# Kernel optimization log

Measured on AMD Instinct MI355X. Metric: run time of the kernel, lower is better.

## Reference

```python
import jax, jax.numpy as jnp
import numpy as np

N = 100000
E = 1600000
IN, HID, OUT = 128, 64, 32


def setup_inputs() -> dict:
    key = jax.random.key(0)
    ks = jax.random.split(key, 8)
    x = jax.random.normal(ks[0], (N, IN), dtype=jnp.float32)
    edge_index = jax.random.randint(ks[1], (2, E), 0, N, dtype=jnp.int32)
    eps = jax.random.normal(ks[2], (N, OUT), dtype=jnp.float32)
    W1 = jax.random.normal(ks[3], (IN, HID), dtype=jnp.float32) / np.sqrt(IN)
    b1 = jnp.zeros((HID,), jnp.float32)
    Wmu = jax.random.normal(ks[4], (HID, OUT), dtype=jnp.float32) / np.sqrt(HID)
    bmu = jnp.zeros((OUT,), jnp.float32)
    Wls = jax.random.normal(ks[5], (HID, OUT), dtype=jnp.float32) / np.sqrt(HID)
    bls = jnp.zeros((OUT,), jnp.float32)
    return dict(x=x, edge_index=edge_index, eps=eps, W1=W1, b1=b1,
                Wmu=Wmu, bmu=bmu, Wls=Wls, bls=bls)


def reference(x, edge_index, eps, W1, b1, Wmu, bmu, Wls, bls):
    n = x.shape[0]
    src, dst = edge_index[0], edge_index[1]
    # GCN with self-loops and symmetric normalization (PyG GCNConv default)
    loop = jnp.arange(n, dtype=src.dtype)
    s = jnp.concatenate([src, loop])   # [E+N]
    d = jnp.concatenate([dst, loop])
    deg = jax.ops.segment_sum(jnp.ones_like(s, jnp.float32), d, num_segments=n)
    dis = jax.lax.rsqrt(jnp.maximum(deg, 1.0))  # deg >= 1 due to self-loops
    norm = dis[s] * dis[d]                       # [E+N]

    def gcn_conv(h, W, b):
        h = h @ W                                # transform first (small dim)
        msg = h[s] * norm[:, None]               # gather over edges
        return jax.ops.segment_sum(msg, d, num_segments=n) + b

    h = jax.nn.relu(gcn_conv(x, W1, b1))
    # F.normalize(h, p=2, dim=-1)
    h = h / jnp.maximum(jnp.linalg.norm(h, axis=-1, keepdims=True), 1e-12)
    mu = gcn_conv(h, Wmu, bmu)
    logstd = gcn_conv(h, Wls, bls)
    # reparametrize (training mode): mu + randn * exp(clamp(logstd, -10, 10))
    z = mu + eps * jnp.exp(jnp.clip(logstd, -10.0, 10.0))
    # decode: sigmoid(<z_i, z_j>) over original edges
    adj_pred = jax.nn.sigmoid(jnp.sum(z[src] * z[dst], axis=1))
    return adj_pred, mu, logstd
```

## Files before the change

### kernel.cpp

```cpp
#include <hip/hip_runtime.h>
#include <hip/hip_fp16.h>

#define NN 100000
#define NE 1600000
#define W_BKT 128
#define NB_BKT ((NN + W_BKT - 1) / W_BKT)
#define TILE_E 16384
#define NT ((NE + TILE_E - 1) / TILE_E)
#define STAGE_CAP 4352

typedef _Float16 half2v __attribute__((ext_vector_type(2)));
typedef _Float16 half8v __attribute__((ext_vector_type(8)));
typedef float float2v __attribute__((ext_vector_type(2)));
typedef float float4v __attribute__((ext_vector_type(4)));


__global__ __launch_bounds__(256) void k_cnt(const int* __restrict__ dst,
                                             int* __restrict__ counts) {
    __shared__ int hc[NB_BKT];
    int tid = threadIdx.x;
    for (int i = tid; i < NB_BKT; i += 256) hc[i] = 0;
    __syncthreads();
    int base = blockIdx.x * TILE_E;
    int lim = base + TILE_E; if (lim > NE) lim = NE;
    for (int e = base + tid; e < lim; e += 256)
        atomicAdd(&hc[dst[e] >> 7], 1);
    __syncthreads();
    for (int i = tid; i < NB_BKT; i += 256)
        counts[blockIdx.x * NB_BKT + i] = hc[i];
}

__global__ __launch_bounds__(1024) void k_bscan(const int* __restrict__ counts,
                                                int* __restrict__ bucket_base) {
    __shared__ int buf[1024];
    int tid = threadIdx.x;
    int total = 0;
    if (tid < NB_BKT)
        for (int t = 0; t < NT; ++t) total += counts[t * NB_BKT + tid];
    buf[tid] = total;
    __syncthreads();
    for (int off = 1; off < 1024; off <<= 1) {
        int v = (tid >= off) ? buf[tid - off] : 0;
        __syncthreads();
        buf[tid] += v;
        __syncthreads();
    }
    if (tid < NB_BKT) bucket_base[tid] = buf[tid] - total;
    if (tid == 0) bucket_base[NB_BKT] = NE;
}

__global__ __launch_bounds__(256) void k_offs(const int* __restrict__ bucket_base,
                                              int* __restrict__ counts) {
    int b = blockIdx.x * 256 + threadIdx.x;
    if (b >= NB_BKT) return;
    int off = bucket_base[b];
    for (int t = 0; t < NT; ++t) {
        int c = counts[t * NB_BKT + b];
        counts[t * NB_BKT + b] = off;
        off += c;
    }
}

__global__ __launch_bounds__(256) void k_place(const int* __restrict__ src,
                                               const int* __restrict__ dst,
                                               const int* __restrict__ counts,
                                               int* __restrict__ ebuf) {
    __shared__ int cur[NB_BKT];
    int tid = threadIdx.x;
    for (int i = tid; i < NB_BKT; i += 256)
        cur[i] = counts[blockIdx.x * NB_BKT + i];
    __syncthreads();
    int base = blockIdx.x * TILE_E;
    int lim = base + TILE_E; if (lim > NE) lim = NE;
    for (int e = base + tid; e < lim; e += 256) {
        int s = src[e], d = dst[e];
        int pos = atomicAdd(&cur[d >> 7], 1);
        ebuf[pos] = (s << 7) | (d & 127);
    }
}

__global__ __launch_bounds__(256) void k_build(const int* __restrict__ bucket_base,
                                               const int* __restrict__ ebuf,
                                               int* __restrict__ csr_src,
                                               int* __restrict__ row_ptr,
                                               float* __restrict__ dis) {
    __shared__ int deg[W_BKT];
    __shared__ int pre[W_BKT];
    __shared__ int cur[W_BKT];
    __shared__ int stage[STAGE_CAP];
    int b = blockIdx.x;
    int tid = threadIdx.x;
    int beg = bucket_base[b], end = bucket_base[b + 1];
    int n = end - beg;
    if (tid < W_BKT) deg[tid] = 0;
    __syncthreads();
    bool fits = (n <= STAGE_CAP);
    if (fits) {
        for (int i = tid; i < n; i += 256) {
            int val = ebuf[beg + i];
            stage[i] = val;
            atomicAdd(&deg[val & 127], 1);
        }
    } else {
        for (int i = tid; i < n; i += 256)
            atomicAdd(&deg[ebuf[beg + i] & 127], 1);
    }
    __syncthreads();
    if (tid < W_BKT) pre[tid] = deg[tid];
    __syncthreads();
    for (int off = 1; off < W_BKT; off <<= 1) {
        int v = (tid >= off && tid < W_BKT) ? pre[tid - off] : 0;
        __syncthreads();
        if (tid < W_BKT) pre[tid] += v;
        __syncthreads();
    }
    if (tid < W_BKT) {
        int v = b * W_BKT + tid;
        int rp = beg + pre[tid] - deg[tid];
        if (v < NN) {
            row_ptr[v] = rp;
            dis[v] = rsqrtf((float)(1 + deg[tid]));
        }
        cur[tid] = rp;
    }
    if (b == NB_BKT - 1 && tid == 0) row_ptr[NN] = NE;
    __syncthreads();
    if (fits) {
        for (int i = tid; i < n; i += 256) {
            int val = stage[i];
            int pos = atomicAdd(&cur[val & 127], 1);
            csr_src[pos] = val >> 7;
        }
    } else {
        for (int i = tid; i < n; i += 256) {
            int val = ebuf[beg + i];
            int pos = atomicAdd(&cur[val & 127], 1);
            csr_src[pos] = val >> 7;
        }
    }
}


__global__ __launch_bounds__(256) void k_wprep(const float* __restrict__ W1,
                                               const float* __restrict__ Wmu,
                                               const float* __restrict__ Wls,
                                               _Float16* __restrict__ wf1h,
                                               _Float16* __restrict__ wf1l,
                                               _Float16* __restrict__ wf2h,
                                               _Float16* __restrict__ wf2l) {
    int tid = threadIdx.x;
    for (int f = tid; f < 4 * 4 * 64; f += 256) {
        int lane = f & 63;
        int kc = (f >> 6) & 3;
        int ct = f >> 8;
        int col = ct * 16 + (lane & 15);
        int k0 = kc * 32 + (lane >> 4) * 8;
#pragma unroll
        for (int j = 0; j < 8; ++j) {
            float w = W1[(k0 + j) * 64 + col];
            _Float16 hi = (_Float16)w;
            wf1h[f * 8 + j] = hi;
            wf1l[f * 8 + j] = (_Float16)(w - (float)hi);
        }
    }
    for (int f = tid; f < 4 * 2 * 64; f += 256) {
        int lane = f & 63;
        int kc = (f >> 6) & 1;
        int ct = f >> 7;
        int col = ct * 16 + (lane & 15);
        int k0 = kc * 32 + (lane >> 4) * 8;
#pragma unroll
        for (int j = 0; j < 8; ++j) {
            int k = k0 + j;
            float w = (col < 32) ? Wmu[k * 32 + col] : Wls[k * 32 + (col - 32)];
            _Float16 hi = (_Float16)w;
            wf2h[f * 8 + j] = hi;
            wf2l[f * 8 + j] = (_Float16)(w - (float)hi);
        }
    }
}

__device__ __forceinline__ void split8(const float4 a, const float4 b,
                                       half8v& hi, half8v& lo) {
    float v[8] = {a.x, a.y, a.z, a.w, b.x, b.y, b.z, b.w};
#pragma unroll
    for (int i = 0; i < 8; ++i) {
        _Float16 h = (_Float16)v[i];
        hi[i] = h;
        lo[i] = (_Float16)(v[i] - (float)h);
    }
}

__global__ __launch_bounds__(256) void k_gemm1(const float* __restrict__ x,
                                               const _Float16* __restrict__ wf1h,
                                               const _Float16* __restrict__ wf1l,
                                               const float* __restrict__ dis,
                                               _Float16* __restrict__ t1) {
    int tid = threadIdx.x;
    int lane = tid & 63;
    int wv = tid >> 6;
    int wrow = blockIdx.x * 64 + wv * 16;
    int cl = lane & 15, kg = lane >> 4;
    const half8v* Bh = (const half8v*)wf1h;
    const half8v* Bl = (const half8v*)wf1l;
    float4v acc[4] = {};
    int r = wrow + cl;
    long rr = (r < NN) ? r : (NN - 1);
    const float4* xp = (const float4*)(x + rr * 128);
#pragma unroll
    for (int kc = 0; kc < 4; ++kc) {
        float4 xa = xp[kc * 8 + kg * 2];
        float4 xb = xp[kc * 8 + kg * 2 + 1];
        half8v ah, al;
        split8(xa, xb, ah, al);
#pragma unroll
        for (int ct = 0; ct < 4; ++ct) {
            half8v bh = Bh[(ct * 4 + kc) * 64 + lane];
            half8v bl = Bl[(ct * 4 + kc) * 64 + lane];
            acc[ct] = __builtin_amdgcn_mfma_f32_16x16x32_f16(ah, bh, acc[ct], 0, 0, 0);
            acc[ct] = __builtin_amdgcn_mfma_f32_16x16x32_f16(al, bh, acc[ct], 0, 0, 0);
            acc[ct] = __builtin_amdgcn_mfma_f32_16x16x32_f16(ah, bl, acc[ct], 0, 0, 0);
        }
    }
#pragma unroll
    for (int j = 0; j < 4; ++j) {
        int row = wrow + kg * 4 + j;
        if (row < NN) {
            float dv = dis[row];
#pragma unroll
            for (int ct = 0; ct < 4; ++ct)
                t1[(long)row * 64 + ct * 16 + cl] = (_Float16)(acc[ct][j] * dv);
        }
    }
}

__global__ __launch_bounds__(256) void k_gemm2(const float* __restrict__ h,
                                               const _Float16* __restrict__ wf2h,
                                               const _Float16* __restrict__ wf2l,
                                               const float* __restrict__ dis,
                                               _Float16* __restrict__ t2) {
    int tid = threadIdx.x;
    int lane = tid & 63;
    int wv = tid >> 6;
    int wrow = blockIdx.x * 64 + wv * 16;
    int cl = lane & 15, kg = lane >> 4;
    const half8v* Bh = (const half8v*)wf2h;
    const half8v* Bl = (const half8v*)wf2l;
    float4v acc[4] = {};
    int r = wrow + cl;
    long rr = (r < NN) ? r : (NN - 1);
    const float4* hp = (const float4*)(h + rr * 64);
#pragma unroll
    for (int kc = 0; kc < 2; ++kc) {
        float4 xa = hp[kc * 8 + kg * 2];
        float4 xb = hp[kc * 8 + kg * 2 + 1];
        half8v ah, al;
        split8(xa, xb, ah, al);
#pragma unroll
        for (int ct = 0; ct < 4; ++ct) {
            half8v bh = Bh[(ct * 2 + kc) * 64 + lane];
            half8v bl = Bl[(ct * 2 + kc) * 64 + lane];
            acc[ct] = __builtin_amdgcn_mfma_f32_16x16x32_f16(ah, bh, acc[ct], 0, 0, 0);
            acc[ct] = __builtin_amdgcn_mfma_f32_16x16x32_f16(al, bh, acc[ct], 0, 0, 0);
            acc[ct] = __builtin_amdgcn_mfma_f32_16x16x32_f16(ah, bl, acc[ct], 0, 0, 0);
        }
    }
#pragma unroll
    for (int j = 0; j < 4; ++j) {
        int row = wrow + kg * 4 + j;
        if (row < NN) {
            float dv = dis[row];
#pragma unroll
            for (int ct = 0; ct < 4; ++ct)
                t2[(long)row * 64 + ct * 16 + cl] = (_Float16)(acc[ct][j] * dv);
        }
    }
}


__global__ __launch_bounds__(256) void k_agg1(const half2v* __restrict__ tv,
                                              const int* __restrict__ row_ptr,
                                              const int* __restrict__ csr_src,
                                              const float* __restrict__ dis,
                                              const float* __restrict__ b1,
                                              float* __restrict__ h) {
    int lane = threadIdx.x & 63;
    int j2 = lane & 31;
    int v = blockIdx.x * 8 + (threadIdx.x >> 6) * 2 + (lane >> 5);
    int beg = row_ptr[v], end = row_ptr[v + 1];
    float acc0 = 0.f, acc1 = 0.f;
    for (int base = beg; base < end; base += 32) {
        int cnt = end - base; if (cnt > 32) cnt = 32;
        int idx = 0;
        if (j2 < cnt) idx = csr_src[base + j2];
        int k = 0;
        for (; k + 8 <= cnt; k += 8) {
            int s0 = __shfl(idx, k, 32),     s1 = __shfl(idx, k + 1, 32),
                s2 = __shfl(idx, k + 2, 32), s3 = __shfl(idx, k + 3, 32),
                s4 = __shfl(idx, k + 4, 32), s5 = __shfl(idx, k + 5, 32),
                s6 = __shfl(idx, k + 6, 32), s7 = __shfl(idx, k + 7, 32);
            half2v r0 = tv[s0 * 32 + j2];
            half2v r1 = tv[s1 * 32 + j2];
            half2v r2 = tv[s2 * 32 + j2];
            half2v r3 = tv[s3 * 32 + j2];
            half2v r4 = tv[s4 * 32 + j2];
            half2v r5 = tv[s5 * 32 + j2];
            half2v r6 = tv[s6 * 32 + j2];
            half2v r7 = tv[s7 * 32 + j2];
            acc0 += (float)r0.x; acc1 += (float)r0.y;
            acc0 += (float)r1.x; acc1 += (float)r1.y;
            acc0 += (float)r2.x; acc1 += (float)r2.y;
            acc0 += (float)r3.x; acc1 += (float)r3.y;
            acc0 += (float)r4.x; acc1 += (float)r4.y;
            acc0 += (float)r5.x; acc1 += (float)r5.y;
            acc0 += (float)r6.x; acc1 += (float)r6.y;
            acc0 += (float)r7.x; acc1 += (float)r7.y;
        }
        for (; k < cnt; ++k) {
            int s = __shfl(idx, k, 32);
            half2v r = tv[s * 32 + j2];
            acc0 += (float)r.x; acc1 += (float)r.y;
        }
    }
    float dv = dis[v];
    half2v rv = tv[v * 32 + j2];
    float val0 = dv * (acc0 + (float)rv.x) + b1[2 * j2];
    float val1 = dv * (acc1 + (float)rv.y) + b1[2 * j2 + 1];
    val0 = fmaxf(val0, 0.0f);
    val1 = fmaxf(val1, 0.0f);
    float ss = val0 * val0 + val1 * val1;
#pragma unroll
    for (int m = 1; m < 32; m <<= 1) ss += __shfl_xor(ss, m);
    float scale = 1.0f / fmaxf(sqrtf(ss), 1e-12f);
    float2v* h2 = (float2v*)h;
    float2v hv; hv.x = val0 * scale; hv.y = val1 * scale;
    h2[v * 32 + j2] = hv;
}

__global__ __launch_bounds__(256) void k_agg2(const half2v* __restrict__ tv,
                                              const int* __restrict__ row_ptr,
                                              const int* __restrict__ csr_src,
                                              const float* __restrict__ dis,
                                              const float* __restrict__ bmu,
                                              const float* __restrict__ bls,
                                              const float* __restrict__ eps,
                                              float* __restrict__ mu,
                                              float* __restrict__ ls,
                                              _Float16* __restrict__ zh) {
    int lane = threadIdx.x & 63;
    int j2 = lane & 31;
    int v = blockIdx.x * 8 + (threadIdx.x >> 6) * 2 + (lane >> 5);
    int beg = row_ptr[v], end = row_ptr[v + 1];
    float acc0 = 0.f, acc1 = 0.f;
    for (int base = beg; base < end; base += 32) {
        int cnt = end - base; if (cnt > 32) cnt = 32;
        int idx = 0;
        if (j2 < cnt) idx = csr_src[base + j2];
        int k = 0;
        for (; k + 8 <= cnt; k += 8) {
            int s0 = __shfl(idx, k, 32),     s1 = __shfl(idx, k + 1, 32),
                s2 = __shfl(idx, k + 2, 32), s3 = __shfl(idx, k + 3, 32),
                s4 = __shfl(idx, k + 4, 32), s5 = __shfl(idx, k + 5, 32),
                s6 = __shfl(idx, k + 6, 32), s7 = __shfl(idx, k + 7, 32);
            half2v r0 = tv[s0 * 32 + j2];
            half2v r1 = tv[s1 * 32 + j2];
            half2v r2 = tv[s2 * 32 + j2];
            half2v r3 = tv[s3 * 32 + j2];
            half2v r4 = tv[s4 * 32 + j2];
            half2v r5 = tv[s5 * 32 + j2];
            half2v r6 = tv[s6 * 32 + j2];
            half2v r7 = tv[s7 * 32 + j2];
            acc0 += (float)r0.x; acc1 += (float)r0.y;
            acc0 += (float)r1.x; acc1 += (float)r1.y;
            acc0 += (float)r2.x; acc1 += (float)r2.y;
            acc0 += (float)r3.x; acc1 += (float)r3.y;
            acc0 += (float)r4.x; acc1 += (float)r4.y;
            acc0 += (float)r5.x; acc1 += (float)r5.y;
            acc0 += (float)r6.x; acc1 += (float)r6.y;
            acc0 += (float)r7.x; acc1 += (float)r7.y;
        }
        for (; k < cnt; ++k) {
            int s = __shfl(idx, k, 32);
            half2v r = tv[s * 32 + j2];
            acc0 += (float)r.x; acc1 += (float)r.y;
        }
    }
    float dv = dis[v];
    half2v rv = tv[v * 32 + j2];
    float bb0 = (j2 < 16) ? bmu[2 * j2]     : bls[2 * j2 - 32];
    float bb1 = (j2 < 16) ? bmu[2 * j2 + 1] : bls[2 * j2 - 31];
    float val0 = dv * (acc0 + (float)rv.x) + bb0;
    float val1 = dv * (acc1 + (float)rv.y) + bb1;
    float o0 = __shfl_xor(val0, 16);
    float o1 = __shfl_xor(val1, 16);
    float2v* mu2 = (float2v*)mu;
    float2v* ls2 = (float2v*)ls;
    half2v* z2  = (half2v*)zh;
    const float2* e2 = (const float2*)eps;
    if (j2 < 16) {
        float2v mv; mv.x = val0; mv.y = val1;
        __builtin_nontemporal_store(mv, &mu2[v * 16 + j2]);
        float2 ev = e2[v * 16 + j2];
        float l0 = fminf(fmaxf(o0, -10.0f), 10.0f);
        float l1 = fminf(fmaxf(o1, -10.0f), 10.0f);
        half2v zw;
        zw.x = (_Float16)(val0 + ev.x * expf(l0));
        zw.y = (_Float16)(val1 + ev.y * expf(l1));
        z2[v * 16 + j2] = zw;
    } else {
        float2v lv; lv.x = val0; lv.y = val1;
        __builtin_nontemporal_store(lv, &ls2[v * 16 + (j2 - 16)]);
    }
}

__global__ __launch_bounds__(256) void k_decode(const _Float16* __restrict__ zh,
                                                const int* __restrict__ src,
                                                const int* __restrict__ dst,
                                                float* __restrict__ out) {
    long t = (long)blockIdx.x * 256 + threadIdx.x;
    long e = t >> 2; int l = (int)(t & 3);
    if (e >= NE) return;
    int s = src[e], d = dst[e];
    const half8v* z8 = (const half8v*)zh;
    half8v a = z8[s * 4 + l];
    half8v b = z8[d * 4 + l];
    float p = 0.f;
#pragma unroll
    for (int i = 0; i < 8; ++i) p += (float)a[i] * (float)b[i];
    p += __shfl_xor(p, 1);
    p += __shfl_xor(p, 2);
    if (l == 0) out[e] = 1.0f / (1.0f + expf(-p));
}

extern "C" void kernel_launch(void* const* d_in, const int* in_sizes, int n_in,
                              void* d_out, int out_size, void* d_ws, size_t ws_size,
                              hipStream_t stream) {
    const float* x   = (const float*)d_in[0];
    const int*   ei  = (const int*)d_in[1];
    const float* eps = (const float*)d_in[2];
    const float* W1  = (const float*)d_in[3];
    const float* b1  = (const float*)d_in[4];
    const float* Wmu = (const float*)d_in[5];
    const float* bmu = (const float*)d_in[6];
    const float* Wls = (const float*)d_in[7];
    const float* bls = (const float*)d_in[8];
    const int* src = ei;
    const int* dst = ei + NE;

    float* out = (float*)d_out;
    float* adj = out;
    float* mu  = out + NE;
    float* ls  = mu + (long)NN * 32;

    float* dis      = (float*)d_ws;
    int*   row_ptr  = (int*)(dis + NN);
    int*   bucket_base = row_ptr + 100004;
    int*   counts   = bucket_base + 784;
    int*   ebuf     = counts + 76640;
    int*   csr_src  = ebuf + NE;
    _Float16* t     = (_Float16*)(csr_src + NE);
    float* h        = (float*)(t + (long)NN * 64);
    _Float16* zh    = (_Float16*)(h + (long)NN * 64 + 12);

    _Float16* wf1h = (_Float16*)counts;
    _Float16* wf1l = wf1h + 8192;
    _Float16* wf2h = wf1l + 8192;
    _Float16* wf2l = wf2h + 4096;

    const int B = 256;

    k_cnt  <<<NT, B, 0, stream>>>(dst, counts);
    k_bscan<<<1, 1024, 0, stream>>>(counts, bucket_base);
    k_offs <<<(NB_BKT + B - 1) / B, B, 0, stream>>>(bucket_base, counts);
    k_place<<<NT, B, 0, stream>>>(src, dst, counts, ebuf);
    k_wprep<<<1, B, 0, stream>>>(W1, Wmu, Wls, wf1h, wf1l, wf2h, wf2l);
    k_build<<<NB_BKT, B, 0, stream>>>(bucket_base, ebuf, csr_src, row_ptr, dis);

    k_gemm1<<<(NN + 63) / 64, B, 0, stream>>>(x, wf1h, wf1l, dis, t);
    k_agg1 <<<NN / 8, B, 0, stream>>>((const half2v*)t, row_ptr, csr_src, dis, b1, h);

    k_gemm2<<<(NN + 63) / 64, B, 0, stream>>>(h, wf2h, wf2l, dis, t);
    k_agg2 <<<NN / 8, B, 0, stream>>>((const half2v*)t, row_ptr, csr_src, dis,
                                      bmu, bls, eps, mu, ls, zh);

    k_decode<<<(int)(((long)NE * 4 + B - 1) / B), B, 0, stream>>>(zh, src, dst, adj);
}
```

Before: 362.9 us.

## Use 16-lane groups with half4 gathers and swizzle broadcast in aggregation

```diff
diff --git a/kernel.cpp b/kernel.cpp
--- a/kernel.cpp
+++ b/kernel.cpp
@@ -10,6 +10,7 @@
 #define STAGE_CAP 4352
 
 typedef _Float16 half2v __attribute__((ext_vector_type(2)));
+typedef _Float16 half4v __attribute__((ext_vector_type(4)));
 typedef _Float16 half8v __attribute__((ext_vector_type(8)));
 typedef float float2v __attribute__((ext_vector_type(2)));
 typedef float float4v __attribute__((ext_vector_type(4)));
@@ -278,66 +279,90 @@
 }
 
 
-__global__ __launch_bounds__(256) void k_agg1(const half2v* __restrict__ tv,
+#define SWZ_LD(K) r[K] = t4[(__builtin_amdgcn_ds_swizzle(idx, ((K) << 5) | 0x10) << 4) + j4];
+
+__device__ __forceinline__ void batch16_full(const half4v* __restrict__ t4, int idx,
+                                             int j4, float* a) {
+    half4v r[16];
+    SWZ_LD(0)  SWZ_LD(1)  SWZ_LD(2)  SWZ_LD(3)
+    SWZ_LD(4)  SWZ_LD(5)  SWZ_LD(6)  SWZ_LD(7)
+    SWZ_LD(8)  SWZ_LD(9)  SWZ_LD(10) SWZ_LD(11)
+    SWZ_LD(12) SWZ_LD(13) SWZ_LD(14) SWZ_LD(15)
+#pragma unroll
+    for (int k = 0; k < 16; ++k) {
+        a[0] += (float)r[k][0]; a[1] += (float)r[k][1];
+        a[2] += (float)r[k][2]; a[3] += (float)r[k][3];
+    }
+}
+
+__device__ __forceinline__ void batch16_mask(const half4v* __restrict__ t4, int idx,
+                                             int j4, int cnt, float* a) {
+    half4v r[16];
+    SWZ_LD(0)  SWZ_LD(1)  SWZ_LD(2)  SWZ_LD(3)
+    SWZ_LD(4)  SWZ_LD(5)  SWZ_LD(6)  SWZ_LD(7)
+    SWZ_LD(8)  SWZ_LD(9)  SWZ_LD(10) SWZ_LD(11)
+    SWZ_LD(12) SWZ_LD(13) SWZ_LD(14) SWZ_LD(15)
+#pragma unroll
+    for (int k = 0; k < 16; ++k) {
+        float w = (k < cnt) ? 1.0f : 0.0f;
+        a[0] += w * (float)r[k][0]; a[1] += w * (float)r[k][1];
+        a[2] += w * (float)r[k][2]; a[3] += w * (float)r[k][3];
+    }
+}
+
+__device__ __forceinline__ void batch8_mask(const half4v* __restrict__ t4, int idx,
+                                            int j4, int cnt, float* a) {
+    half4v r[8];
+    SWZ_LD(0)  SWZ_LD(1)  SWZ_LD(2)  SWZ_LD(3)
+    SWZ_LD(4)  SWZ_LD(5)  SWZ_LD(6)  SWZ_LD(7)
+#pragma unroll
+    for (int k = 0; k < 8; ++k) {
+        float w = (k < cnt) ? 1.0f : 0.0f;
+        a[0] += w * (float)r[k][0]; a[1] += w * (float)r[k][1];
+        a[2] += w * (float)r[k][2]; a[3] += w * (float)r[k][3];
+    }
+}
+
+__global__ __launch_bounds__(256) void k_agg1(const half4v* __restrict__ tv4,
                                               const int* __restrict__ row_ptr,
                                               const int* __restrict__ csr_src,
                                               const float* __restrict__ dis,
                                               const float* __restrict__ b1,
                                               float* __restrict__ h) {
     int lane = threadIdx.x & 63;
-    int j2 = lane & 31;
-    int v = blockIdx.x * 8 + (threadIdx.x >> 6) * 2 + (lane >> 5);
+    int j4 = lane & 15;
+    int v = blockIdx.x * 16 + (threadIdx.x >> 6) * 4 + (lane >> 4);
     int beg = row_ptr[v], end = row_ptr[v + 1];
-    float acc0 = 0.f, acc1 = 0.f;
-    for (int base = beg; base < end; base += 32) {
-        int cnt = end - base; if (cnt > 32) cnt = 32;
-        int idx = 0;
-        if (j2 < cnt) idx = csr_src[base + j2];
-        int k = 0;
-        for (; k + 8 <= cnt; k += 8) {
-            int s0 = __shfl(idx, k, 32),     s1 = __shfl(idx, k + 1, 32),
-                s2 = __shfl(idx, k + 2, 32), s3 = __shfl(idx, k + 3, 32),
-                s4 = __shfl(idx, k + 4, 32), s5 = __shfl(idx, k + 5, 32),
-                s6 = __shfl(idx, k + 6, 32), s7 = __shfl(idx, k + 7, 32);
-            half2v r0 = tv[s0 * 32 + j2];
-            half2v r1 = tv[s1 * 32 + j2];
-            half2v r2 = tv[s2 * 32 + j2];
-            half2v r3 = tv[s3 * 32 + j2];
-            half2v r4 = tv[s4 * 32 + j2];
-            half2v r5 = tv[s5 * 32 + j2];
-            half2v r6 = tv[s6 * 32 + j2];
-            half2v r7 = tv[s7 * 32 + j2];
-            acc0 += (float)r0.x; acc1 += (float)r0.y;
-            acc0 += (float)r1.x; acc1 += (float)r1.y;
-            acc0 += (float)r2.x; acc1 += (float)r2.y;
-            acc0 += (float)r3.x; acc1 += (float)r3.y;
-            acc0 += (float)r4.x; acc1 += (float)r4.y;
-            acc0 += (float)r5.x; acc1 += (float)r5.y;
-            acc0 += (float)r6.x; acc1 += (float)r6.y;
-            acc0 += (float)r7.x; acc1 += (float)r7.y;
-        }
-        for (; k < cnt; ++k) {
-            int s = __shfl(idx, k, 32);
-            half2v r = tv[s * 32 + j2];
-            acc0 += (float)r.x; acc1 += (float)r.y;
-        }
+    float a[4] = {0.f, 0.f, 0.f, 0.f};
+    int base = beg;
+    for (; base + 16 <= end; base += 16) {
+        int idx = csr_src[base + j4];
+        batch16_full(tv4, idx, j4, a);
+    }
+    int cnt = end - base;
+    if (cnt > 0) {
+        int idx = csr_src[base + ((j4 < cnt) ? j4 : cnt - 1)];
+        if (cnt > 8) batch16_mask(tv4, idx, j4, cnt, a);
+        else         batch8_mask(tv4, idx, j4, cnt, a);
     }
     float dv = dis[v];
-    half2v rv = tv[v * 32 + j2];
-    float val0 = dv * (acc0 + (float)rv.x) + b1[2 * j2];
-    float val1 = dv * (acc1 + (float)rv.y) + b1[2 * j2 + 1];
-    val0 = fmaxf(val0, 0.0f);
-    val1 = fmaxf(val1, 0.0f);
-    float ss = val0 * val0 + val1 * val1;
-#pragma unroll
-    for (int m = 1; m < 32; m <<= 1) ss += __shfl_xor(ss, m);
+    half4v rv = tv4[(v << 4) + j4];
+    float4 bb = ((const float4*)b1)[j4];
+    float val0 = fmaxf(dv * (a[0] + (float)rv[0]) + bb.x, 0.0f);
+    float val1 = fmaxf(dv * (a[1] + (float)rv[1]) + bb.y, 0.0f);
+    float val2 = fmaxf(dv * (a[2] + (float)rv[2]) + bb.z, 0.0f);
+    float val3 = fmaxf(dv * (a[3] + (float)rv[3]) + bb.w, 0.0f);
+    float ss = val0 * val0 + val1 * val1 + val2 * val2 + val3 * val3;
+#pragma unroll
+    for (int m = 1; m < 16; m <<= 1) ss += __shfl_xor(ss, m);
     float scale = 1.0f / fmaxf(sqrtf(ss), 1e-12f);
-    float2v* h2 = (float2v*)h;
-    float2v hv; hv.x = val0 * scale; hv.y = val1 * scale;
-    h2[v * 32 + j2] = hv;
-}
-
-__global__ __launch_bounds__(256) void k_agg2(const half2v* __restrict__ tv,
+    float4v* h4 = (float4v*)h;
+    float4v hv; hv.x = val0 * scale; hv.y = val1 * scale;
+    hv.z = val2 * scale; hv.w = val3 * scale;
+    h4[(v << 4) + j4] = hv;
+}
+
+__global__ __launch_bounds__(256) void k_agg2(const half4v* __restrict__ tv4,
                                               const int* __restrict__ row_ptr,
                                               const int* __restrict__ csr_src,
                                               const float* __restrict__ dis,
@@ -348,68 +373,53 @@
                                               float* __restrict__ ls,
                                               _Float16* __restrict__ zh) {
     int lane = threadIdx.x & 63;
-    int j2 = lane & 31;
-    int v = blockIdx.x * 8 + (threadIdx.x >> 6) * 2 + (lane >> 5);
+    int j4 = lane & 15;
+    int v = blockIdx.x * 16 + (threadIdx.x >> 6) * 4 + (lane >> 4);
     int beg = row_ptr[v], end = row_ptr[v + 1];
-    float acc0 = 0.f, acc1 = 0.f;
-    for (int base = beg; base < end; base += 32) {
-        int cnt = end - base; if (cnt > 32) cnt = 32;
-        int idx = 0;
-        if (j2 < cnt) idx = csr_src[base + j2];
-        int k = 0;
-        for (; k + 8 <= cnt; k += 8) {
-            int s0 = __shfl(idx, k, 32),     s1 = __shfl(idx, k + 1, 32),
-                s2 = __shfl(idx, k + 2, 32), s3 = __shfl(idx, k + 3, 32),
-                s4 = __shfl(idx, k + 4, 32), s5 = __shfl(idx, k + 5, 32),
-                s6 = __shfl(idx, k + 6, 32), s7 = __shfl(idx, k + 7, 32);
-            half2v r0 = tv[s0 * 32 + j2];
-            half2v r1 = tv[s1 * 32 + j2];
-            half2v r2 = tv[s2 * 32 + j2];
-            half2v r3 = tv[s3 * 32 + j2];
-            half2v r4 = tv[s4 * 32 + j2];
-            half2v r5 = tv[s5 * 32 + j2];
-            half2v r6 = tv[s6 * 32 + j2];
-            half2v r7 = tv[s7 * 32 + j2];
-            acc0 += (float)r0.x; acc1 += (float)r0.y;
-            acc0 += (float)r1.x; acc1 += (float)r1.y;
-            acc0 += (float)r2.x; acc1 += (float)r2.y;
-            acc0 += (float)r3.x; acc1 += (float)r3.y;
-            acc0 += (float)r4.x; acc1 += (float)r4.y;
-            acc0 += (float)r5.x; acc1 += (float)r5.y;
-            acc0 += (float)r6.x; acc1 += (float)r6.y;
-            acc0 += (float)r7.x; acc1 += (float)r7.y;
-        }
-        for (; k < cnt; ++k) {
-            int s = __shfl(idx, k, 32);
-            half2v r = tv[s * 32 + j2];
-            acc0 += (float)r.x; acc1 += (float)r.y;
-        }
+    float a[4] = {0.f, 0.f, 0.f, 0.f};
+    int base = beg;
+    for (; base + 16 <= end; base += 16) {
+        int idx = csr_src[base + j4];
+        batch16_full(tv4, idx, j4, a);
+    }
+    int cnt = end - base;
+    if (cnt > 0) {
+        int idx = csr_src[base + ((j4 < cnt) ? j4 : cnt - 1)];
+        if (cnt > 8) batch16_mask(tv4, idx, j4, cnt, a);
+        else         batch8_mask(tv4, idx, j4, cnt, a);
     }
     float dv = dis[v];
-    half2v rv = tv[v * 32 + j2];
-    float bb0 = (j2 < 16) ? bmu[2 * j2]     : bls[2 * j2 - 32];
-    float bb1 = (j2 < 16) ? bmu[2 * j2 + 1] : bls[2 * j2 - 31];
-    float val0 = dv * (acc0 + (float)rv.x) + bb0;
-    float val1 = dv * (acc1 + (float)rv.y) + bb1;
-    float o0 = __shfl_xor(val0, 16);
-    float o1 = __shfl_xor(val1, 16);
-    float2v* mu2 = (float2v*)mu;
-    float2v* ls2 = (float2v*)ls;
-    half2v* z2  = (half2v*)zh;
-    const float2* e2 = (const float2*)eps;
-    if (j2 < 16) {
-        float2v mv; mv.x = val0; mv.y = val1;
-        __builtin_nontemporal_store(mv, &mu2[v * 16 + j2]);
-        float2 ev = e2[v * 16 + j2];
+    half4v rv = tv4[(v << 4) + j4];
+    float4 bb = (j4 < 8) ? ((const float4*)bmu)[j4] : ((const float4*)bls)[j4 - 8];
+    float val0 = dv * (a[0] + (float)rv[0]) + bb.x;
+    float val1 = dv * (a[1] + (float)rv[1]) + bb.y;
+    float val2 = dv * (a[2] + (float)rv[2]) + bb.z;
+    float val3 = dv * (a[3] + (float)rv[3]) + bb.w;
+    float o0 = __shfl_xor(val0, 8);
+    float o1 = __shfl_xor(val1, 8);
+    float o2 = __shfl_xor(val2, 8);
+    float o3 = __shfl_xor(val3, 8);
+    float4v* mu4 = (float4v*)mu;
+    float4v* ls4 = (float4v*)ls;
+    half4v* z4  = (half4v*)zh;
+    const float4* e4 = (const float4*)eps;
+    if (j4 < 8) {
+        float4v mv; mv.x = val0; mv.y = val1; mv.z = val2; mv.w = val3;
+        __builtin_nontemporal_store(mv, &mu4[(v << 3) + j4]);
+        float4 ev = e4[(v << 3) + j4];
         float l0 = fminf(fmaxf(o0, -10.0f), 10.0f);
         float l1 = fminf(fmaxf(o1, -10.0f), 10.0f);
-        half2v zw;
-        zw.x = (_Float16)(val0 + ev.x * expf(l0));
-        zw.y = (_Float16)(val1 + ev.y * expf(l1));
-        z2[v * 16 + j2] = zw;
+        float l2 = fminf(fmaxf(o2, -10.0f), 10.0f);
+        float l3 = fminf(fmaxf(o3, -10.0f), 10.0f);
+        half4v zw;
+        zw[0] = (_Float16)(val0 + ev.x * expf(l0));
+        zw[1] = (_Float16)(val1 + ev.y * expf(l1));
+        zw[2] = (_Float16)(val2 + ev.z * expf(l2));
+        zw[3] = (_Float16)(val3 + ev.w * expf(l3));
+        z4[(v << 3) + j4] = zw;
     } else {
-        float2v lv; lv.x = val0; lv.y = val1;
-        __builtin_nontemporal_store(lv, &ls2[v * 16 + (j2 - 16)]);
+        float4v lv; lv.x = val0; lv.y = val1; lv.z = val2; lv.w = val3;
+        __builtin_nontemporal_store(lv, &ls4[(v << 3) + (j4 - 8)]);
     }
 }
 
@@ -477,11 +487,11 @@
     k_build<<<NB_BKT, B, 0, stream>>>(bucket_base, ebuf, csr_src, row_ptr, dis);
 
     k_gemm1<<<(NN + 63) / 64, B, 0, stream>>>(x, wf1h, wf1l, dis, t);
-    k_agg1 <<<NN / 8, B, 0, stream>>>((const half2v*)t, row_ptr, csr_src, dis, b1, h);
+    k_agg1 <<<NN / 16, B, 0, stream>>>((const half4v*)t, row_ptr, csr_src, dis, b1, h);
 
     k_gemm2<<<(NN + 63) / 64, B, 0, stream>>>(h, wf2h, wf2l, dis, t);
-    k_agg2 <<<NN / 8, B, 0, stream>>>((const half2v*)t, row_ptr, csr_src, dis,
-                                      bmu, bls, eps, mu, ls, zh);
+    k_agg2 <<<NN / 16, B, 0, stream>>>((const half4v*)t, row_ptr, csr_src, dis,
+                                       bmu, bls, eps, mu, ls, zh);
 
     k_decode<<<(int)(((long)NE * 4 + B - 1) / B), B, 0, stream>>>(zh, src, dst, adj);
 }
```

Measured after the change: 348.4 us, median of 2. 4.0% less time.
